# Kernel optimization log

Measured on AMD Instinct MI355X. Metric: run time of the kernel, lower is better.

## Reference

```python
import jax, jax.numpy as jnp
import numpy as np
from jax.scipy.special import xlogy

W_BI = 0.5
W_TRI = 0.5
EPS = 1e-10


def setup_inputs() -> dict:
    key = jax.random.key(0)
    B, L, V = 8, 2048, 512
    logits = jax.random.normal(key, (B, L, V), dtype=jnp.float32)
    return {"logits": logits}


def _safe_normalized_entropy(joint, max_log):
    # 1 - H(joint)/H_max (concentration penalty), fp32-safe
    joint = joint / (joint.sum() + EPS)
    entropy = -xlogy(joint, jnp.clip(joint, EPS, None)).sum()
    return jnp.clip(1.0 - entropy / (max_log + EPS), 0.0, 1.0)


def reference(logits):
    x = jnp.nan_to_num(logits.astype(jnp.float32), nan=0.0, posinf=80.0, neginf=-80.0)
    p = jax.nn.softmax(x, axis=-1)  # (B, L, V)
    B, L, V = p.shape
    max_log_bi = float(np.log(float(V * V)))
    max_log_tri = float(np.log(float(V) ** 3))

    total = jnp.zeros((), dtype=jnp.float32)

    # Bigram joint distribution over (V, V)
    bigram_joint = jnp.einsum('nla,nlb->ab', p[:, :-1, :], p[:, 1:, :])
    total = total + W_BI * _safe_normalized_entropy(bigram_joint, max_log_bi)

    # Trigram: (V,V) bigram part outer-producted with third-position marginal -> (V,V,V)
    bi_part = jnp.einsum('nla,nlb->ab', p[:, :-2, :], p[:, 1:-1, :])
    tri_joint = jnp.einsum('ab,nlc->abc', bi_part, p[:, 2:, :])
    total = total + W_TRI * _safe_normalized_entropy(tri_joint, max_log_tri)

    return jnp.clip(jnp.nan_to_num(total, nan=0.0, posinf=1.0), 0.0, 1.0)
```

## Files before the change

### kernel.cpp

```cpp
#include <hip/hip_runtime.h>
#include <math.h>

#define L_SEQ 2048
#define V 512
#define NROWS 16384
#define LDT 16448
#define NSPLIT 32
#define EPS 1e-10

typedef __bf16 bf16x8 __attribute__((ext_vector_type(8)));
typedef float f32x4 __attribute__((ext_vector_type(4)));

#define PT_OFF  ((size_t)0)
#define GP_OFF  ((size_t)512 * LDT * 2)
#define RB_OFF  (GP_OFF + (size_t)NSPLIT * V * V * 4)
#define M_OFF   (RB_OFF + (size_t)23 * V * 4)
#define PC_OFF  (M_OFF + (size_t)V * 4)

#define GLDS16(g, l) __builtin_amdgcn_global_load_lds( \
    (const __attribute__((address_space(1))) unsigned int*)(g), \
    (__attribute__((address_space(3))) unsigned int*)(l), 16, 0, 0)

__device__ __forceinline__ unsigned short f2bf(float f) {
    unsigned u = __float_as_uint(f);
    unsigned r = (u + 0x7fffu + ((u >> 16) & 1u)) >> 16;
    return (unsigned short)r;
}

__device__ __forceinline__ void softmax_row_bf16(const float* __restrict__ x,
                                                 int lane, unsigned short* out) {
    float4 va = *(const float4*)(x + lane * 4);
    float4 vb = *(const float4*)(x + 256 + lane * 4);
    float v[8] = {va.x, va.y, va.z, va.w, vb.x, vb.y, vb.z, vb.w};
#pragma unroll
    for (int i = 0; i < 8; i++) {
        float xi = v[i];
        if (isnan(xi)) xi = 0.0f;
        else if (isinf(xi)) xi = xi > 0.0f ? 80.0f : -80.0f;
        v[i] = xi;
    }
    float mx = v[0];
#pragma unroll
    for (int i = 1; i < 8; i++) mx = fmaxf(mx, v[i]);
#pragma unroll
    for (int o = 32; o; o >>= 1) mx = fmaxf(mx, __shfl_xor(mx, o, 64));
    float e[8];
    float s = 0.0f;
#pragma unroll
    for (int i = 0; i < 8; i++) { e[i] = expf(v[i] - mx); s += e[i]; }
#pragma unroll
    for (int o = 32; o; o >>= 1) s += __shfl_xor(s, o, 64);
    float inv = 1.0f / s;
#pragma unroll
    for (int i = 0; i < 8; i++) out[i] = f2bf(e[i] * inv);
}

__global__ __launch_bounds__(256) void softmaxT_k(const float* __restrict__ in,
                                                  unsigned short* __restrict__ pT) {
    __shared__ __align__(16) unsigned short sm[16 * 512];
    int t = threadIdx.x;
    int w = t >> 6, lane = t & 63;
    int k0 = blockIdx.x * 16;
#pragma unroll
    for (int i = 0; i < 4; i++) {
        int rr = w * 4 + i;
        unsigned short o[8];
        softmax_row_bf16(in + (size_t)(k0 + rr) * V, lane, o);
        *(ushort4*)&sm[rr * 512 + lane * 4] = make_ushort4(o[0], o[1], o[2], o[3]);
        *(ushort4*)&sm[rr * 512 + 256 + lane * 4] = make_ushort4(o[4], o[5], o[6], o[7]);
    }
    __syncthreads();
    int cA = 2 * t, cB = cA + 1;
    unsigned u[16];
#pragma unroll
    for (int k = 0; k < 16; k++) u[k] = *(const unsigned*)&sm[k * 512 + cA];
    unsigned oA[8], oB[8];
#pragma unroll
    for (int i = 0; i < 8; i++) {
        unsigned e0 = u[2 * i], e1 = u[2 * i + 1];
        oA[i] = (e0 & 0xffffu) | (e1 << 16);
        oB[i] = (e0 >> 16) | (e1 & 0xffff0000u);
    }
    uint4* dA = (uint4*)(pT + (size_t)cA * LDT + k0);
    uint4* dB = (uint4*)(pT + (size_t)cB * LDT + k0);
    dA[0] = make_uint4(oA[0], oA[1], oA[2], oA[3]);
    dA[1] = make_uint4(oA[4], oA[5], oA[6], oA[7]);
    dB[0] = make_uint4(oB[0], oB[1], oB[2], oB[3]);
    dB[1] = make_uint4(oB[4], oB[5], oB[6], oB[7]);
    if (blockIdx.x == 1023) {
#pragma unroll
        for (int j = 0; j < 8; j++) {
            *(uint4*)(pT + (size_t)cA * LDT + 16384 + 8 * j) = make_uint4(0, 0, 0, 0);
            *(uint4*)(pT + (size_t)cB * LDT + 16384 + 8 * j) = make_uint4(0, 0, 0, 0);
        }
    }
}

__global__ __launch_bounds__(64) void rows_k(const float* __restrict__ in,
                                             float* __restrict__ rb) {
    int j = blockIdx.x, lane = threadIdx.x;
    int r = j < 8 ? j * L_SEQ + L_SEQ - 2
          : j < 16 ? (j - 8) * L_SEQ + L_SEQ - 1
          : (j - 15) * L_SEQ;
    unsigned short o[8];
    softmax_row_bf16(in + (size_t)r * V, lane, o);
#pragma unroll
    for (int i = 0; i < 4; i++)
        rb[j * V + lane * 4 + i] = __uint_as_float((unsigned)o[i] << 16);
#pragma unroll
    for (int i = 0; i < 4; i++)
        rb[j * V + 256 + lane * 4 + i] = __uint_as_float((unsigned)o[4 + i] << 16);
}

__global__ __launch_bounds__(256) void colsum_k(const unsigned short* __restrict__ pT,
                                                float* __restrict__ m) {
    int c = blockIdx.x, t = threadIdx.x;
    const unsigned short* row = pT + (size_t)c * LDT;
    float s = 0.0f;
#pragma unroll
    for (int j = 0; j < 8; j++) {
        int g = t + 256 * j;
        uint4 x = *(const uint4*)(row + g * 8);
        float partial = 0.0f;
        unsigned ww[4] = {x.x, x.y, x.z, x.w};
#pragma unroll
        for (int qq = 0; qq < 4; qq++) {
            partial += __uint_as_float(ww[qq] << 16);
            partial += __uint_as_float(ww[qq] & 0xffff0000u);
        }
        if ((g & 255) == 0)
            partial -= __uint_as_float(ww[0] << 16) + __uint_as_float(ww[0] & 0xffff0000u);
        s += partial;
    }
#pragma unroll
    for (int o = 32; o; o >>= 1) s += __shfl_xor(s, o, 64);
    __shared__ float red[4];
    if ((t & 63) == 0) red[t >> 6] = s;
    __syncthreads();
    if (t == 0) m[c] = red[0] + red[1] + red[2] + red[3];
}

__global__ __launch_bounds__(256) void gemm_k(const unsigned short* __restrict__ pT,
                                              float* __restrict__ gp) {
    __shared__ __align__(16) uint4 ldsA[512];
    __shared__ __align__(16) uint4 ldsB[512];
    int tile = blockIdx.x & 15, split = blockIdx.x >> 4;
    int ta = (tile >> 2) * 128, tb = (tile & 3) * 128;
    int t = threadIdx.x, w = t >> 6, lane = t & 63;
    int l15 = lane & 15, q = lane >> 4;
    int wa = (w & 1) * 64, wb = (w >> 1) * 64;
    int k0base = split * 512;

    f32x4 acc[4][4];
#pragma unroll
    for (int g = 0; g < 4; g++)
#pragma unroll
        for (int h = 0; h < 4; h++) acc[g][h] = (f32x4){0.f, 0.f, 0.f, 0.f};

    int srow = 16 * w + (lane >> 2);
    int qoff = (lane & 3) * 8;
    const size_t rA1 = (size_t)(ta + srow) * LDT;
    const size_t rA2 = (size_t)(ta + 64 + srow) * LDT;
    const size_t rB1 = (size_t)(tb + srow) * LDT;
    const size_t rB2 = (size_t)(tb + 64 + srow) * LDT;

    for (int it = 0; it < 16; it++) {
        int kel = k0base + it * 32 + qoff;
        const unsigned short* gb1 = pT + rB1 + kel;
        const unsigned short* gb2 = pT + rB2 + kel;
        uint4 x1 = *(const uint4*)gb1;
        unsigned y1 = *(const unsigned*)(gb1 + 8);
        uint4 x2 = *(const uint4*)gb2;
        unsigned y2 = *(const unsigned*)(gb2 + 8);
        __syncthreads();
        GLDS16(pT + rA1 + kel, &ldsA[64 * w]);
        GLDS16(pT + rA2 + kel, &ldsA[256 + 64 * w]);
        uint4 s1, s2;
        s1.x = (x1.x >> 16) | (x1.y << 16);
        s1.y = (x1.y >> 16) | (x1.z << 16);
        s1.z = (x1.z >> 16) | (x1.w << 16);
        s1.w = (x1.w >> 16) | (y1 << 16);
        s2.x = (x2.x >> 16) | (x2.y << 16);
        s2.y = (x2.y >> 16) | (x2.z << 16);
        s2.z = (x2.z >> 16) | (x2.w << 16);
        s2.w = (x2.w >> 16) | (y2 << 16);
        ldsB[64 * w + lane] = s1;
        ldsB[256 + 64 * w + lane] = s2;
        __syncthreads();
        bf16x8 af[4], bv[4];
#pragma unroll
        for (int g = 0; g < 4; g++)
            af[g] = __builtin_bit_cast(bf16x8, ldsA[4 * (wa + g * 16 + l15) + q]);
#pragma unroll
        for (int h = 0; h < 4; h++)
            bv[h] = __builtin_bit_cast(bf16x8, ldsB[4 * (wb + h * 16 + l15) + q]);
#pragma unroll
        for (int g = 0; g < 4; g++)
#pragma unroll
            for (int h = 0; h < 4; h++)
                acc[g][h] = __builtin_amdgcn_mfma_f32_16x16x32_bf16(af[g], bv[h], acc[g][h], 0, 0, 0);
    }

    float* og = gp + (size_t)split * V * V;
#pragma unroll
    for (int g = 0; g < 4; g++) {
        int a = ta + wa + g * 16 + q * 4;
#pragma unroll
        for (int h = 0; h < 4; h++) {
            int b = tb + wb + h * 16 + l15;
#pragma unroll
            for (int r = 0; r < 4; r++)
                og[(size_t)(a + r) * V + b] = acc[g][h][r];
        }
    }
}

__global__ __launch_bounds__(256) void reduceg_k(const float* __restrict__ gp,
                                                 const float* __restrict__ rb,
                                                 double* __restrict__ pc) {
    int t = threadIdx.x;
    int idx = blockIdx.x * 256 + t;
    int a = idx >> 9, b = idx & (V - 1);
    double ga = 0, gb2 = 0, gc = 0, gd = 0;
#pragma unroll
    for (int s = 0; s < NSPLIT; s += 4) {
        ga += (double)gp[(size_t)(s + 0) * V * V + idx];
        gb2 += (double)gp[(size_t)(s + 1) * V * V + idx];
        gc += (double)gp[(size_t)(s + 2) * V * V + idx];
        gd += (double)gp[(size_t)(s + 3) * V * V + idx];
    }
    double g = (ga + gb2) + (gc + gd);
    float cross = 0.f, cc = 0.f;
#pragma unroll
    for (int n = 0; n < 7; n++)
        cross = fmaf(rb[(8 + n) * V + a], rb[(16 + n) * V + b], cross);
#pragma unroll
    for (int n = 0; n < 8; n++)
        cc = fmaf(rb[n * V + a], rb[(8 + n) * V + b], cc);
    double g1 = g - (double)cross;
    double g2 = g1 - (double)cc;
    double s1 = g1, t1 = g1 * (double)logf((float)g1);
    double s2 = g2, t2 = g2 * (double)logf((float)g2);
#pragma unroll
    for (int o = 32; o; o >>= 1) {
        s1 += __shfl_xor(s1, o, 64);
        t1 += __shfl_xor(t1, o, 64);
        s2 += __shfl_xor(s2, o, 64);
        t2 += __shfl_xor(t2, o, 64);
    }
    __shared__ double red[4][4];
    if ((t & 63) == 0) {
        int w = t >> 6;
        red[w][0] = s1; red[w][1] = t1; red[w][2] = s2; red[w][3] = t2;
    }
    __syncthreads();
    if (t == 0) {
        double* o = pc + (size_t)blockIdx.x * 4;
        o[0] = red[0][0] + red[1][0] + red[2][0] + red[3][0];
        o[1] = red[0][1] + red[1][1] + red[2][1] + red[3][1];
        o[2] = red[0][2] + red[1][2] + red[2][2] + red[3][2];
        o[3] = red[0][3] + red[1][3] + red[2][3] + red[3][3];
    }
}

__global__ __launch_bounds__(512) void final_k(const float* __restrict__ m,
                                               const double* __restrict__ pc,
                                               float* __restrict__ out) {
    int t = threadIdx.x;
    double s1 = 0, t1 = 0, s2 = 0, t2 = 0;
#pragma unroll
    for (int j = 0; j < 2; j++) {
        const double* q = pc + (size_t)(t + 512 * j) * 4;
        s1 += q[0]; t1 += q[1]; s2 += q[2]; t2 += q[3];
    }
    double mv = (double)m[t];
    double sm = mv;
    double tm = mv * log(mv);
#pragma unroll
    for (int o = 32; o; o >>= 1) {
        sm += __shfl_xor(sm, o, 64);
        tm += __shfl_xor(tm, o, 64);
        s1 += __shfl_xor(s1, o, 64);
        t1 += __shfl_xor(t1, o, 64);
        s2 += __shfl_xor(s2, o, 64);
        t2 += __shfl_xor(t2, o, 64);
    }
    __shared__ double red[6][8];
    if ((t & 63) == 0) {
        int w = t >> 6;
        red[0][w] = sm; red[1][w] = tm;
        red[2][w] = s1; red[3][w] = t1;
        red[4][w] = s2; red[5][w] = t2;
    }
    __syncthreads();
    if (t == 0) {
        double acc[6];
        for (int i = 0; i < 6; i++) {
            acc[i] = 0;
            for (int w = 0; w < 8; w++) acc[i] += red[i][w];
        }
        double Sm = acc[0], Tm = acc[1];
        double S1 = acc[2], T1 = acc[3], S2 = acc[4], T2 = acc[5];
        double D1 = S1 + EPS;
        double Hbi = (log(D1) * S1 - T1) / D1;
        double mlb = log((double)V * (double)V);
        double cbi = 1.0 - Hbi / (mlb + EPS);
        cbi = fmin(fmax(cbi, 0.0), 1.0);
        double S3 = S2 * Sm;
        double D3 = S3 + EPS;
        double Htri = (log(D3) * S3 - (Sm * T2 + S2 * Tm)) / D3;
        double mlt = log((double)V * (double)V * (double)V);
        double ctri = 1.0 - Htri / (mlt + EPS);
        ctri = fmin(fmax(ctri, 0.0), 1.0);
        double tot = 0.5 * cbi + 0.5 * ctri;
        if (!(tot == tot)) tot = 0.0;
        tot = fmin(fmax(tot, 0.0), 1.0);
        out[0] = (float)tot;
    }
}

extern "C" void kernel_launch(void* const* d_in, const int* in_sizes, int n_in,
                              void* d_out, int out_size, void* d_ws, size_t ws_size,
                              hipStream_t stream) {
    (void)in_sizes; (void)n_in; (void)out_size; (void)ws_size;
    const float* logits = (const float*)d_in[0];
    float* out = (float*)d_out;
    char* ws = (char*)d_ws;
    unsigned short* pT = (unsigned short*)(ws + PT_OFF);
    float* gp = (float*)(ws + GP_OFF);
    float* rb = (float*)(ws + RB_OFF);
    float* m = (float*)(ws + M_OFF);
    double* pc = (double*)(ws + PC_OFF);

    softmaxT_k<<<1024, 256, 0, stream>>>(logits, pT);
    rows_k<<<23, 64, 0, stream>>>(logits, rb);
    colsum_k<<<512, 256, 0, stream>>>(pT, m);
    gemm_k<<<512, 256, 0, stream>>>(pT, gp);
    reduceg_k<<<1024, 256, 0, stream>>>(gp, rb, pc);
    final_k<<<1, 512, 0, stream>>>(m, pc, out);
}
```

Before: 120.5 us.

## Fuse kernels into three launches and halve GEMM split-K partials

Folds the boundary-row softmax into extra blocks of the softmax/transpose kernel. Merges colsum, split-K reduction and the final scalar reduction into one kernel that uses an atomic counter so the last block finishes. Halves the split-K count, giving each GEMM block twice the K range, which halves the partial-sum traffic. This removes three launches and their gaps, but the GEMM now runs only 256 blocks, which may underfill the GPU, and the last-block pattern adds atomics and fences.

```diff
diff --git a/kernel.cpp b/kernel.cpp
--- a/kernel.cpp
+++ b/kernel.cpp
@@ -5,7 +5,7 @@
 #define V 512
 #define NROWS 16384
 #define LDT 16448
-#define NSPLIT 32
+#define NSPLIT 16
 #define EPS 1e-10
 
 typedef __bf16 bf16x8 __attribute__((ext_vector_type(8)));
@@ -16,6 +16,7 @@
 #define RB_OFF  (GP_OFF + (size_t)NSPLIT * V * V * 4)
 #define M_OFF   (RB_OFF + (size_t)23 * V * 4)
 #define PC_OFF  (M_OFF + (size_t)V * 4)
+#define CTR_OFF (PC_OFF + (size_t)1024 * 4 * 8)
 
 #define GLDS16(g, l) __builtin_amdgcn_global_load_lds( \
     (const __attribute__((address_space(1))) unsigned int*)(g), \
@@ -56,10 +57,30 @@
 }
 
 __global__ __launch_bounds__(256) void softmaxT_k(const float* __restrict__ in,
-                                                  unsigned short* __restrict__ pT) {
+                                                  unsigned short* __restrict__ pT,
+                                                  float* __restrict__ rb,
+                                                  unsigned* __restrict__ ctr) {
     __shared__ __align__(16) unsigned short sm[16 * 512];
     int t = threadIdx.x;
     int w = t >> 6, lane = t & 63;
+    if (blockIdx.x >= 1024) {
+        int j = blockIdx.x - 1024;
+        if (j == 0 && t == 0) *ctr = 0;
+        if (w == 0) {
+            int r = j < 8 ? j * L_SEQ + L_SEQ - 2
+                  : j < 16 ? (j - 8) * L_SEQ + L_SEQ - 1
+                  : (j - 15) * L_SEQ;
+            unsigned short o[8];
+            softmax_row_bf16(in + (size_t)r * V, lane, o);
+#pragma unroll
+            for (int i = 0; i < 4; i++)
+                rb[j * V + lane * 4 + i] = __uint_as_float((unsigned)o[i] << 16);
+#pragma unroll
+            for (int i = 0; i < 4; i++)
+                rb[j * V + 256 + lane * 4 + i] = __uint_as_float((unsigned)o[4 + i] << 16);
+        }
+        return;
+    }
     int k0 = blockIdx.x * 16;
 #pragma unroll
     for (int i = 0; i < 4; i++) {
@@ -94,50 +115,6 @@
             *(uint4*)(pT + (size_t)cB * LDT + 16384 + 8 * j) = make_uint4(0, 0, 0, 0);
         }
     }
-}
-
-__global__ __launch_bounds__(64) void rows_k(const float* __restrict__ in,
-                                             float* __restrict__ rb) {
-    int j = blockIdx.x, lane = threadIdx.x;
-    int r = j < 8 ? j * L_SEQ + L_SEQ - 2
-          : j < 16 ? (j - 8) * L_SEQ + L_SEQ - 1
-          : (j - 15) * L_SEQ;
-    unsigned short o[8];
-    softmax_row_bf16(in + (size_t)r * V, lane, o);
-#pragma unroll
-    for (int i = 0; i < 4; i++)
-        rb[j * V + lane * 4 + i] = __uint_as_float((unsigned)o[i] << 16);
-#pragma unroll
-    for (int i = 0; i < 4; i++)
-        rb[j * V + 256 + lane * 4 + i] = __uint_as_float((unsigned)o[4 + i] << 16);
-}
-
-__global__ __launch_bounds__(256) void colsum_k(const unsigned short* __restrict__ pT,
-                                                float* __restrict__ m) {
-    int c = blockIdx.x, t = threadIdx.x;
-    const unsigned short* row = pT + (size_t)c * LDT;
-    float s = 0.0f;
-#pragma unroll
-    for (int j = 0; j < 8; j++) {
-        int g = t + 256 * j;
-        uint4 x = *(const uint4*)(row + g * 8);
-        float partial = 0.0f;
-        unsigned ww[4] = {x.x, x.y, x.z, x.w};
-#pragma unroll
-        for (int qq = 0; qq < 4; qq++) {
-            partial += __uint_as_float(ww[qq] << 16);
-            partial += __uint_as_float(ww[qq] & 0xffff0000u);
-        }
-        if ((g & 255) == 0)
-            partial -= __uint_as_float(ww[0] << 16) + __uint_as_float(ww[0] & 0xffff0000u);
-        s += partial;
-    }
-#pragma unroll
-    for (int o = 32; o; o >>= 1) s += __shfl_xor(s, o, 64);
-    __shared__ float red[4];
-    if ((t & 63) == 0) red[t >> 6] = s;
-    __syncthreads();
-    if (t == 0) m[c] = red[0] + red[1] + red[2] + red[3];
 }
 
 __global__ __launch_bounds__(256) void gemm_k(const unsigned short* __restrict__ pT,
@@ -149,7 +126,7 @@
     int t = threadIdx.x, w = t >> 6, lane = t & 63;
     int l15 = lane & 15, q = lane >> 4;
     int wa = (w & 1) * 64, wb = (w >> 1) * 64;
-    int k0base = split * 512;
+    int k0base = split * 1024;
 
     f32x4 acc[4][4];
 #pragma unroll
@@ -164,7 +141,7 @@
     const size_t rB1 = (size_t)(tb + srow) * LDT;
     const size_t rB2 = (size_t)(tb + 64 + srow) * LDT;
 
-    for (int it = 0; it < 16; it++) {
+    for (int it = 0; it < 32; it++) {
         int kel = k0base + it * 32 + qoff;
         const unsigned short* gb1 = pT + rB1 + kel;
         const unsigned short* gb2 = pT + rB2 + kel;
@@ -215,67 +192,100 @@
     }
 }
 
-__global__ __launch_bounds__(256) void reduceg_k(const float* __restrict__ gp,
-                                                 const float* __restrict__ rb,
-                                                 double* __restrict__ pc) {
-    int t = threadIdx.x;
-    int idx = blockIdx.x * 256 + t;
-    int a = idx >> 9, b = idx & (V - 1);
-    double ga = 0, gb2 = 0, gc = 0, gd = 0;
-#pragma unroll
-    for (int s = 0; s < NSPLIT; s += 4) {
-        ga += (double)gp[(size_t)(s + 0) * V * V + idx];
-        gb2 += (double)gp[(size_t)(s + 1) * V * V + idx];
-        gc += (double)gp[(size_t)(s + 2) * V * V + idx];
-        gd += (double)gp[(size_t)(s + 3) * V * V + idx];
-    }
-    double g = (ga + gb2) + (gc + gd);
-    float cross = 0.f, cc = 0.f;
-#pragma unroll
-    for (int n = 0; n < 7; n++)
-        cross = fmaf(rb[(8 + n) * V + a], rb[(16 + n) * V + b], cross);
-#pragma unroll
-    for (int n = 0; n < 8; n++)
-        cc = fmaf(rb[n * V + a], rb[(8 + n) * V + b], cc);
-    double g1 = g - (double)cross;
-    double g2 = g1 - (double)cc;
-    double s1 = g1, t1 = g1 * (double)logf((float)g1);
-    double s2 = g2, t2 = g2 * (double)logf((float)g2);
-#pragma unroll
-    for (int o = 32; o; o >>= 1) {
-        s1 += __shfl_xor(s1, o, 64);
-        t1 += __shfl_xor(t1, o, 64);
-        s2 += __shfl_xor(s2, o, 64);
-        t2 += __shfl_xor(t2, o, 64);
-    }
-    __shared__ double red[4][4];
-    if ((t & 63) == 0) {
-        int w = t >> 6;
-        red[w][0] = s1; red[w][1] = t1; red[w][2] = s2; red[w][3] = t2;
-    }
+__global__ __launch_bounds__(256) void reduce_all_k(const unsigned short* __restrict__ pT,
+                                                    const float* __restrict__ gp,
+                                                    const float* __restrict__ rb,
+                                                    float* __restrict__ m,
+                                                    double* __restrict__ pc,
+                                                    unsigned* __restrict__ ctr,
+                                                    float* __restrict__ out) {
+    int bid = blockIdx.x, t = threadIdx.x;
+    if (bid < 512) {
+        const unsigned short* row = pT + (size_t)bid * LDT;
+        float s = 0.0f;
+#pragma unroll
+        for (int j = 0; j < 8; j++) {
+            int g = t + 256 * j;
+            uint4 x = *(const uint4*)(row + g * 8);
+            float partial = 0.0f;
+            unsigned ww[4] = {x.x, x.y, x.z, x.w};
+#pragma unroll
+            for (int qq = 0; qq < 4; qq++) {
+                partial += __uint_as_float(ww[qq] << 16);
+                partial += __uint_as_float(ww[qq] & 0xffff0000u);
+            }
+            if ((g & 255) == 0)
+                partial -= __uint_as_float(ww[0] << 16) + __uint_as_float(ww[0] & 0xffff0000u);
+            s += partial;
+        }
+#pragma unroll
+        for (int o = 32; o; o >>= 1) s += __shfl_xor(s, o, 64);
+        __shared__ float redc[4];
+        if ((t & 63) == 0) redc[t >> 6] = s;
+        __syncthreads();
+        if (t == 0) m[bid] = redc[0] + redc[1] + redc[2] + redc[3];
+    } else {
+        int idx = (bid - 512) * 256 + t;
+        int a = idx >> 9, b = idx & (V - 1);
+        double ga = 0, gb2 = 0, gc = 0, gd = 0;
+#pragma unroll
+        for (int s = 0; s < NSPLIT; s += 4) {
+            ga += (double)gp[(size_t)(s + 0) * V * V + idx];
+            gb2 += (double)gp[(size_t)(s + 1) * V * V + idx];
+            gc += (double)gp[(size_t)(s + 2) * V * V + idx];
+            gd += (double)gp[(size_t)(s + 3) * V * V + idx];
+        }
+        double g = (ga + gb2) + (gc + gd);
+        float cross = 0.f, cc = 0.f;
+#pragma unroll
+        for (int n = 0; n < 7; n++)
+            cross = fmaf(rb[(8 + n) * V + a], rb[(16 + n) * V + b], cross);
+#pragma unroll
+        for (int n = 0; n < 8; n++)
+            cc = fmaf(rb[n * V + a], rb[(8 + n) * V + b], cc);
+        double g1 = g - (double)cross;
+        double g2 = g1 - (double)cc;
+        double s1 = g1, t1 = g1 * (double)logf((float)g1);
+        double s2 = g2, t2 = g2 * (double)logf((float)g2);
+#pragma unroll
+        for (int o = 32; o; o >>= 1) {
+            s1 += __shfl_xor(s1, o, 64);
+            t1 += __shfl_xor(t1, o, 64);
+            s2 += __shfl_xor(s2, o, 64);
+            t2 += __shfl_xor(t2, o, 64);
+        }
+        __shared__ double redg[4][4];
+        if ((t & 63) == 0) {
+            int w = t >> 6;
+            redg[w][0] = s1; redg[w][1] = t1; redg[w][2] = s2; redg[w][3] = t2;
+        }
+        __syncthreads();
+        if (t == 0) {
+            double* o = pc + (size_t)(bid - 512) * 4;
+            o[0] = redg[0][0] + redg[1][0] + redg[2][0] + redg[3][0];
+            o[1] = redg[0][1] + redg[1][1] + redg[2][1] + redg[3][1];
+            o[2] = redg[0][2] + redg[1][2] + redg[2][2] + redg[3][2];
+            o[3] = redg[0][3] + redg[1][3] + redg[2][3] + redg[3][3];
+        }
+    }
+    __threadfence();
+    __shared__ int isLast;
+    if (t == 0) isLast = (atomicAdd(ctr, 1u) == 1535u) ? 1 : 0;
     __syncthreads();
-    if (t == 0) {
-        double* o = pc + (size_t)blockIdx.x * 4;
-        o[0] = red[0][0] + red[1][0] + red[2][0] + red[3][0];
-        o[1] = red[0][1] + red[1][1] + red[2][1] + red[3][1];
-        o[2] = red[0][2] + red[1][2] + red[2][2] + red[3][2];
-        o[3] = red[0][3] + red[1][3] + red[2][3] + red[3][3];
-    }
-}
-
-__global__ __launch_bounds__(512) void final_k(const float* __restrict__ m,
-                                               const double* __restrict__ pc,
-                                               float* __restrict__ out) {
-    int t = threadIdx.x;
-    double s1 = 0, t1 = 0, s2 = 0, t2 = 0;
+    if (!isLast) return;
+    __threadfence();
+    double s1 = 0, t1 = 0, s2 = 0, t2 = 0, sm = 0, tm = 0;
+#pragma unroll
+    for (int j = 0; j < 4; j++) {
+        const double* q = pc + (size_t)(t + 256 * j) * 4;
+        s1 += q[0]; t1 += q[1]; s2 += q[2]; t2 += q[3];
+    }
 #pragma unroll
     for (int j = 0; j < 2; j++) {
-        const double* q = pc + (size_t)(t + 512 * j) * 4;
-        s1 += q[0]; t1 += q[1]; s2 += q[2]; t2 += q[3];
-    }
-    double mv = (double)m[t];
-    double sm = mv;
-    double tm = mv * log(mv);
+        double mv = (double)m[t + 256 * j];
+        sm += mv;
+        tm += mv * log(mv);
+    }
 #pragma unroll
     for (int o = 32; o; o >>= 1) {
         sm += __shfl_xor(sm, o, 64);
@@ -285,7 +295,7 @@
         s2 += __shfl_xor(s2, o, 64);
         t2 += __shfl_xor(t2, o, 64);
     }
-    __shared__ double red[6][8];
+    __shared__ double red[6][4];
     if ((t & 63) == 0) {
         int w = t >> 6;
         red[0][w] = sm; red[1][w] = tm;
@@ -295,10 +305,8 @@
     __syncthreads();
     if (t == 0) {
         double acc[6];
-        for (int i = 0; i < 6; i++) {
-            acc[i] = 0;
-            for (int w = 0; w < 8; w++) acc[i] += red[i][w];
-        }
+        for (int i = 0; i < 6; i++)
+            acc[i] = red[i][0] + red[i][1] + red[i][2] + red[i][3];
         double Sm = acc[0], Tm = acc[1];
         double S1 = acc[2], T1 = acc[3], S2 = acc[4], T2 = acc[5];
         double D1 = S1 + EPS;
@@ -331,11 +339,9 @@
     float* rb = (float*)(ws + RB_OFF);
     float* m = (float*)(ws + M_OFF);
     double* pc = (double*)(ws + PC_OFF);
-
-    softmaxT_k<<<1024, 256, 0, stream>>>(logits, pT);
-    rows_k<<<23, 64, 0, stream>>>(logits, rb);
-    colsum_k<<<512, 256, 0, stream>>>(pT, m);
-    gemm_k<<<512, 256, 0, stream>>>(pT, gp);
-    reduceg_k<<<1024, 256, 0, stream>>>(gp, rb, pc);
-    final_k<<<1, 512, 0, stream>>>(m, pc, out);
-}
+    unsigned* ctr = (unsigned*)(ws + CTR_OFF);
+
+    softmaxT_k<<<1047, 256, 0, stream>>>(logits, pT, rb, ctr);
+    gemm_k<<<256, 256, 0, stream>>>(pT, gp);
+    reduce_all_k<<<1536, 256, 0, stream>>>(pT, gp, rb, m, pc, ctr, out);
+}
```

New measurement: 235.8 us. 95.6% more time.
